# Kernel optimization log

Hardware: AMD Instinct MI355X
Metric: run time of the kernel (lower is better)

Reference implementation:

```python
import jax, jax.numpy as jnp
import numpy as np

N_NODES = 100000
N_EDGES = 3_200_000
F_IN, HID, N_CLS = 512, 16, 16


def setup_inputs() -> dict:
    key = jax.random.key(0)
    k1, k2, k3, k4 = jax.random.split(key, 4)
    x = jax.random.normal(k1, (N_NODES, F_IN), dtype=jnp.float32)
    edge_index = jax.random.randint(k2, (2, N_EDGES), 0, N_NODES, dtype=jnp.int64)
    W1 = jax.random.normal(k3, (F_IN, HID), dtype=jnp.float32) * 0.05
    b1 = jnp.zeros((HID,), dtype=jnp.float32)
    W2 = jax.random.normal(k4, (HID, N_CLS), dtype=jnp.float32) * 0.05
    b2 = jnp.zeros((N_CLS,), dtype=jnp.float32)
    return {"x": x, "edge_index": edge_index, "W1": W1, "b1": b1, "W2": W2, "b2": b2}


def _gcn_conv(x, W, b, row, col, norm, n_nodes):
    # GCNConv: linear first, then symmetric-normalized scatter-add aggregation
    h = x @ W                              # [N, out]
    msg = h[row] * norm[:, None]           # gather + scale, [E+N, out]
    out = jax.ops.segment_sum(msg, col, num_segments=n_nodes)
    return out + b


def reference(x, edge_index, W1, b1, W2, b2):
    n = x.shape[0]
    # add self-loops (GCNConv default)
    loop = jnp.arange(n, dtype=edge_index.dtype)
    row = jnp.concatenate([edge_index[0], loop])
    col = jnp.concatenate([edge_index[1], loop])
    # symmetric normalization D^-1/2 A D^-1/2 with edge_weight = 1
    deg = jax.ops.segment_sum(jnp.ones_like(col, dtype=x.dtype), col, num_segments=n)
    dinv = jnp.where(deg > 0, deg ** -0.5, 0.0)
    norm = dinv[row] * dinv[col]

    h = jax.nn.relu(_gcn_conv(x, W1, b1, row, col, norm, n))
    # dropout is identity in eval mode
    out = _gcn_conv(h, W2, b2, row, col, norm, n)
    return jax.nn.log_softmax(out, axis=-1)
```

## Files before the change

kernel.cpp:

```cpp
#include <hip/hip_runtime.h>
#include <hip/hip_fp16.h>

#define F_IN 512
#define BKT_BITS 7
#define NPB (1 << BKT_BITS)
#define NBMAX 1024
#define BWIN 5120
#define EPT 16
#define EPW (256 * EPT)

__global__ void k_init(int* __restrict__ cursor, int nb) {
    int i = blockIdx.x * blockDim.x + threadIdx.x;
    if (i < nb) cursor[i] = i * BWIN;
}

__global__ __launch_bounds__(256) void k_part(
    const int* __restrict__ row, const int* __restrict__ col,
    int* __restrict__ cursor, unsigned int* __restrict__ pairs, int E, int nb)
{
    __shared__ int hist[NBMAX];
    __shared__ int base[NBMAX];
    int tid = threadIdx.x;
    int e0 = blockIdx.x * EPW;
    for (int i = tid; i < nb; i += 256) hist[i] = 0;
    __syncthreads();
    int4 c4[EPT / 4];
    int rank[EPT];
    #pragma unroll
    for (int k = 0; k < EPT / 4; ++k) {
        int e = e0 + (tid + k * 256) * 4;
        if (e + 3 < E) {
            c4[k] = ((const int4*)col)[e >> 2];
        } else {
            c4[k].x = (e     < E) ? col[e]     : -1;
            c4[k].y = (e + 1 < E) ? col[e + 1] : -1;
            c4[k].z = (e + 2 < E) ? col[e + 2] : -1;
            c4[k].w = (e + 3 < E) ? col[e + 3] : -1;
        }
        const int* cc = (const int*)&c4[k];
        #pragma unroll
        for (int i = 0; i < 4; ++i)
            rank[4 * k + i] = (cc[i] >= 0) ? atomicAdd(&hist[cc[i] >> BKT_BITS], 1) : 0;
    }
    __syncthreads();
    for (int i = tid; i < nb; i += 256)
        base[i] = hist[i] ? atomicAdd(&cursor[i], hist[i]) : 0;
    __syncthreads();
    #pragma unroll
    for (int k = 0; k < EPT / 4; ++k) {
        int e = e0 + (tid + k * 256) * 4;
        int4 r4;
        if (e + 3 < E) {
            r4 = ((const int4*)row)[e >> 2];
        } else {
            r4.x = (e     < E) ? row[e]     : 0;
            r4.y = (e + 1 < E) ? row[e + 1] : 0;
            r4.z = (e + 2 < E) ? row[e + 2] : 0;
            r4.w = (e + 3 < E) ? row[e + 3] : 0;
        }
        const int* cc = (const int*)&c4[k];
        const int* rr = (const int*)&r4;
        #pragma unroll
        for (int i = 0; i < 4; ++i) {
            if (e + i >= E || cc[i] < 0) continue;
            int b = cc[i] >> BKT_BITS;
            int slot = b * BWIN + min(rank[4 * k + i] +
                       (int)0, BWIN - 1);
            slot = b * BWIN;
            int s2 = slot + (base[b] - slot) + rank[4 * k + i];
            if (s2 < (b + 1) * BWIN)
                pairs[s2] = ((unsigned int)rr[i] << BKT_BITS)
                          | (unsigned int)(cc[i] & (NPB - 1));
        }
    }
}

__global__ __launch_bounds__(256) void k_csr(
    unsigned int* __restrict__ pairs, const int* __restrict__ cursor,
    int2* __restrict__ pd, float* __restrict__ dinv, int n, int nb)
{
    __shared__ int hist[NPB];
    __shared__ int sc[NPB];
    __shared__ int curs[NPB];
    int b = blockIdx.x, tid = threadIdx.x;
    int n0 = b << BKT_BITS;
    int w0 = b * BWIN;
    int ec = min(cursor[b] - w0, BWIN);
    if (tid < NPB) hist[tid] = 0;
    __syncthreads();
    uint4 pv4[BWIN / 1024];
    #pragma unroll
    for (int k = 0; k < BWIN / 1024; ++k) {
        pv4[k] = ((const uint4*)(pairs + w0))[tid + k * 256];
        int e = (tid + k * 256) * 4;
        const unsigned int* pp = (const unsigned int*)&pv4[k];
        #pragma unroll
        for (int i = 0; i < 4; ++i)
            if (e + i < ec) atomicAdd(&hist[pp[i] & (NPB - 1)], 1);
    }
    __syncthreads();
    if (tid < NPB) sc[tid] = hist[tid];
    __syncthreads();
    for (int off = 1; off < NPB; off <<= 1) {
        int t = (tid < NPB && tid >= off) ? sc[tid - off] : 0;
        __syncthreads();
        if (tid < NPB) sc[tid] += t;
        __syncthreads();
    }
    if (tid < NPB) {
        int st = sc[tid] - hist[tid];
        curs[tid] = st;
        int node = n0 + tid;
        if (node < n) {
            pd[node] = make_int2(w0 + st, hist[tid]);
            dinv[node] = rsqrtf((float)(hist[tid] + 1));
        }
    }
    __syncthreads();
    #pragma unroll
    for (int k = 0; k < BWIN / 1024; ++k) {
        int e = (tid + k * 256) * 4;
        const unsigned int* pp = (const unsigned int*)&pv4[k];
        #pragma unroll
        for (int i = 0; i < 4; ++i) {
            if (e + i < ec) {
                unsigned int p = pp[i];
                int pos = atomicAdd(&curs[p & (NPB - 1)], 1);
                ((int*)pairs)[w0 + pos] = (int)(p >> BKT_BITS);
            }
        }
    }
}

__global__ __launch_bounds__(256) void k_gemm1(
    const float* __restrict__ x, const float* __restrict__ W1,
    const float* __restrict__ dinv, __half2* __restrict__ hs, int n)
{
    __shared__ float red[4][64 * 17];
    const int lane = threadIdx.x & 63;
    const int wib  = threadIdx.x >> 6;
    const int wave = blockIdx.x * 4 + wib;
    const int nw   = gridDim.x * 4;
    float* rb = red[wib];

    float w[128];
    #pragma unroll
    for (int i = 0; i < 32; ++i) {
        float4 t = ((const float4*)W1)[lane * 32 + i];
        w[4*i+0] = t.x; w[4*i+1] = t.y; w[4*i+2] = t.z; w[4*i+3] = t.w;
    }
    const int q  = lane >> 4;
    const int jj = lane & 15;

    int node = wave;
    float4 a = {}, b = {};
    float di = 0.f;
    if (node < n) {
        const float4* xr = (const float4*)(x + (size_t)node * F_IN);
        a = xr[lane * 2];
        b = xr[lane * 2 + 1];
        di = dinv[node];
    }
    while (node < n) {
        int nxt = node + nw;
        float4 an = {}, bn = {};
        float dn = 0.f;
        if (nxt < n) {
            const float4* xr = (const float4*)(x + (size_t)nxt * F_IN);
            an = xr[lane * 2];
            bn = xr[lane * 2 + 1];
            dn = dinv[nxt];
        }
        float xs[8] = {a.x, a.y, a.z, a.w, b.x, b.y, b.z, b.w};
        float p[16];
        #pragma unroll
        for (int j = 0; j < 16; ++j) p[j] = 0.f;
        #pragma unroll
        for (int i = 0; i < 8; ++i)
            #pragma unroll
            for (int j = 0; j < 16; ++j)
                p[j] = fmaf(xs[i], w[i * 16 + j], p[j]);

        #pragma unroll
        for (int j = 0; j < 16; ++j) rb[lane * 17 + j] = p[j];
        __asm__ volatile("s_waitcnt lgkmcnt(0)" ::: "memory");
        float s = 0.f;
        #pragma unroll
        for (int i = 0; i < 16; ++i) s += rb[(q * 16 + i) * 17 + jj];
        s += __shfl_down(s, 32);
        s += __shfl_down(s, 16);

        float sv = s * di;
        float sn = __shfl_down(sv, 1);
        if (lane < 16 && (lane & 1) == 0) {
            __half2 hv = __halves2half2(__float2half(sv), __float2half(sn));
            hs[node * 8 + (lane >> 1)] = hv;
        }
        node = nxt; a = an; b = bn; di = dn;
    }
}

__global__ __launch_bounds__(256) void k_agg1(
    const __half2* __restrict__ hs, const int2* __restrict__ pd,
    const int* __restrict__ csr, const float* __restrict__ dinv,
    const float* __restrict__ b1, const float* __restrict__ W2,
    __half2* __restrict__ hs2, int n)
{
    int t = blockIdx.x * blockDim.x + threadIdx.x;
    int node = t >> 3, j2 = t & 7;
    if (node >= n) return;
    int2 p = pd[node];
    int e = p.x, s1 = p.x + p.y;
    float2 sum = __half22float2(hs[node * 8 + j2]);
    for (; e + 8 <= s1; e += 8) {
        int a0 = csr[e],   a1 = csr[e+1], a2 = csr[e+2], a3 = csr[e+3];
        int a4 = csr[e+4], a5 = csr[e+5], a6 = csr[e+6], a7 = csr[e+7];
        float2 v0 = __half22float2(hs[a0 * 8 + j2]);
        float2 v1 = __half22float2(hs[a1 * 8 + j2]);
        float2 v2 = __half22float2(hs[a2 * 8 + j2]);
        float2 v3 = __half22float2(hs[a3 * 8 + j2]);
        float2 v4 = __half22float2(hs[a4 * 8 + j2]);
        float2 v5 = __half22float2(hs[a5 * 8 + j2]);
        float2 v6 = __half22float2(hs[a6 * 8 + j2]);
        float2 v7 = __half22float2(hs[a7 * 8 + j2]);
        sum.x += ((v0.x+v1.x)+(v2.x+v3.x)) + ((v4.x+v5.x)+(v6.x+v7.x));
        sum.y += ((v0.y+v1.y)+(v2.y+v3.y)) + ((v4.y+v5.y)+(v6.y+v7.y));
    }
    for (; e < s1; ++e) {
        float2 v = __half22float2(hs[csr[e] * 8 + j2]);
        sum.x += v.x; sum.y += v.y;
    }
    float di = dinv[node];
    float2 b1v = ((const float2*)b1)[j2];
    float va = fmaxf(fmaf(sum.x, di, b1v.x), 0.f);
    float vb = fmaxf(fmaf(sum.y, di, b1v.y), 0.f);
    float ha = 0.f, hb = 0.f;
    #pragma unroll
    for (int k2 = 0; k2 < 8; ++k2) {
        float oa = __shfl(va, k2, 8);
        float ob = __shfl(vb, k2, 8);
        ha = fmaf(oa, W2[(2*k2)   * 16 + 2*j2],     ha);
        hb = fmaf(oa, W2[(2*k2)   * 16 + 2*j2 + 1], hb);
        ha = fmaf(ob, W2[(2*k2+1) * 16 + 2*j2],     ha);
        hb = fmaf(ob, W2[(2*k2+1) * 16 + 2*j2 + 1], hb);
    }
    hs2[node * 8 + j2] = __halves2half2(__float2half(ha * di), __float2half(hb * di));
}

__global__ __launch_bounds__(256) void k_agg2(
    const __half2* __restrict__ hs2, const int2* __restrict__ pd,
    const int* __restrict__ csr, const float* __restrict__ dinv,
    const float* __restrict__ b2, float2* __restrict__ out, int n)
{
    int t = blockIdx.x * blockDim.x + threadIdx.x;
    int node = t >> 3, j2 = t & 7;
    if (node >= n) return;
    int2 p = pd[node];
    int e = p.x, s1 = p.x + p.y;
    float2 sum = __half22float2(hs2[node * 8 + j2]);
    for (; e + 8 <= s1; e += 8) {
        int a0 = csr[e],   a1 = csr[e+1], a2 = csr[e+2], a3 = csr[e+3];
        int a4 = csr[e+4], a5 = csr[e+5], a6 = csr[e+6], a7 = csr[e+7];
        float2 v0 = __half22float2(hs2[a0 * 8 + j2]);
        float2 v1 = __half22float2(hs2[a1 * 8 + j2]);
        float2 v2 = __half22float2(hs2[a2 * 8 + j2]);
        float2 v3 = __half22float2(hs2[a3 * 8 + j2]);
        float2 v4 = __half22float2(hs2[a4 * 8 + j2]);
        float2 v5 = __half22float2(hs2[a5 * 8 + j2]);
        float2 v6 = __half22float2(hs2[a6 * 8 + j2]);
        float2 v7 = __half22float2(hs2[a7 * 8 + j2]);
        sum.x += ((v0.x+v1.x)+(v2.x+v3.x)) + ((v4.x+v5.x)+(v6.x+v7.x));
        sum.y += ((v0.y+v1.y)+(v2.y+v3.y)) + ((v4.y+v5.y)+(v6.y+v7.y));
    }
    for (; e < s1; ++e) {
        float2 v = __half22float2(hs2[csr[e] * 8 + j2]);
        sum.x += v.x; sum.y += v.y;
    }
    float di = dinv[node];
    float2 b2v = ((const float2*)b2)[j2];
    float vx = fmaf(sum.x, di, b2v.x);
    float vy = fmaf(sum.y, di, b2v.y);
    float m = fmaxf(vx, vy);
    #pragma unroll
    for (int off = 4; off >= 1; off >>= 1) m = fmaxf(m, __shfl_xor(m, off));
    float s = expf(vx - m) + expf(vy - m);
    #pragma unroll
    for (int off = 4; off >= 1; off >>= 1) s += __shfl_xor(s, off);
    float ls = logf(s);
    out[node * 8 + j2] = make_float2(vx - m - ls, vy - m - ls);
}

extern "C" void kernel_launch(void* const* d_in, const int* in_sizes, int n_in,
                              void* d_out, int out_size, void* d_ws, size_t ws_size,
                              hipStream_t stream)
{
    const float* x  = (const float*)d_in[0];
    const int*   ei = (const int*)d_in[1];
    const float* W1 = (const float*)d_in[2];
    const float* b1 = (const float*)d_in[3];
    const float* W2 = (const float*)d_in[4];
    const float* b2 = (const float*)d_in[5];
    float* out = (float*)d_out;

    const int n = in_sizes[0] / F_IN;
    const int E = in_sizes[1] / 2;
    const int nb = (n + NPB - 1) >> BKT_BITS;

    char* ws = (char*)d_ws;
    size_t o = 0;
    #define ALIGN512(s) (((s) + 511) & ~(size_t)511)
    float* dinv = (float*)(ws + o);           o += ALIGN512((size_t)n * 4);
    int2*  pd   = (int2*)(ws + o);            o += ALIGN512((size_t)n * 8);
    int*   curs = (int*)(ws + o);             o += ALIGN512((size_t)NBMAX * 4);
    unsigned int* pairs = (unsigned int*)(ws + o);
    o += ALIGN512((size_t)nb * BWIN * 4);
    __half2* hs  = (__half2*)(ws + o);        o += ALIGN512((size_t)n * 16 * 2);
    __half2* hs2 = (__half2*)(ws + o);        o += ALIGN512((size_t)n * 16 * 2);
    #undef ALIGN512

    k_init<<<(nb + 255) / 256, 256, 0, stream>>>(curs, nb);
    k_part<<<(E + EPW - 1) / EPW, 256, 0, stream>>>(ei, ei + E, curs, pairs, E, nb);
    k_csr <<<nb, 256, 0, stream>>>(pairs, curs, pd, dinv, n, nb);

    k_gemm1<<<2048, 256, 0, stream>>>(x, W1, dinv, hs, n);
    k_agg1 <<<(n * 8 + 255) / 256, 256, 0, stream>>>(hs, pd, (const int*)pairs,
                                                     dinv, b1, W2, hs2, n);
    k_agg2 <<<(n * 8 + 255) / 256, 256, 0, stream>>>(hs2, pd, (const int*)pairs,
                                                     dinv, b2, (float2*)out, n);
}
```

Before: 465.5 us.

## Stage partition scatter in LDS and assign a wave per node in aggregation

The partition kernel now processes twice as many edges per block. Each block first sorts its edges by bucket in shared memory using a 1024-entry prefix scan, then writes each bucket's run to global memory as a contiguous span instead of scattering individual words. The CSR kernel builds its sorted window in LDS and writes it back linearly rather than scattering into global memory. Both aggregation kernels now use 64 threads per node, splitting edges across 8 slots and reducing with shuffles. This raises parallelism for the gathers but idles most lanes on low-degree nodes and adds LDS and shuffle overhead.

```diff
diff --git a/kernel.cpp b/kernel.cpp
--- a/kernel.cpp
+++ b/kernel.cpp
@@ -6,7 +6,7 @@
 #define NPB (1 << BKT_BITS)
 #define NBMAX 1024
 #define BWIN 5120
-#define EPT 16
+#define EPT 32
 #define EPW (256 * EPT)
 
 __global__ void k_init(int* __restrict__ cursor, int nb) {
@@ -18,12 +18,16 @@
     const int* __restrict__ row, const int* __restrict__ col,
     int* __restrict__ cursor, unsigned int* __restrict__ pairs, int E, int nb)
 {
+    __shared__ unsigned int staged[EPW];
+    __shared__ unsigned short bkt[EPW];
     __shared__ int hist[NBMAX];
+    __shared__ int sc[NBMAX];
     __shared__ int base[NBMAX];
     int tid = threadIdx.x;
     int e0 = blockIdx.x * EPW;
     for (int i = tid; i < nb; i += 256) hist[i] = 0;
     __syncthreads();
+
     int4 c4[EPT / 4];
     int rank[EPT];
     #pragma unroll
@@ -43,9 +47,23 @@
             rank[4 * k + i] = (cc[i] >= 0) ? atomicAdd(&hist[cc[i] >> BKT_BITS], 1) : 0;
     }
     __syncthreads();
-    for (int i = tid; i < nb; i += 256)
-        base[i] = hist[i] ? atomicAdd(&cursor[i], hist[i]) : 0;
-    __syncthreads();
+
+    for (int i = tid; i < NBMAX; i += 256) {
+        int h = (i < nb) ? hist[i] : 0;
+        base[i] = h ? atomicAdd(&cursor[i], h) : 0;
+        sc[i] = h;
+    }
+    __syncthreads();
+    for (int off = 1; off < NBMAX; off <<= 1) {
+        int t0 = (tid       >= off) ? sc[tid       - off] : 0;
+        int t1 = (tid + 256 >= off) ? sc[tid + 256 - off] : 0;
+        int t2 = (tid + 512 >= off) ? sc[tid + 512 - off] : 0;
+        int t3 = (tid + 768 >= off) ? sc[tid + 768 - off] : 0;
+        __syncthreads();
+        sc[tid] += t0; sc[tid + 256] += t1; sc[tid + 512] += t2; sc[tid + 768] += t3;
+        __syncthreads();
+    }
+
     #pragma unroll
     for (int k = 0; k < EPT / 4; ++k) {
         int e = e0 + (tid + k * 256) * 4;
@@ -64,14 +82,20 @@
         for (int i = 0; i < 4; ++i) {
             if (e + i >= E || cc[i] < 0) continue;
             int b = cc[i] >> BKT_BITS;
-            int slot = b * BWIN + min(rank[4 * k + i] +
-                       (int)0, BWIN - 1);
-            slot = b * BWIN;
-            int s2 = slot + (base[b] - slot) + rank[4 * k + i];
-            if (s2 < (b + 1) * BWIN)
-                pairs[s2] = ((unsigned int)rr[i] << BKT_BITS)
-                          | (unsigned int)(cc[i] & (NPB - 1));
-        }
+            int pos = (sc[b] - hist[b]) + rank[4 * k + i];
+            staged[pos] = ((unsigned int)rr[i] << BKT_BITS)
+                        | (unsigned int)(cc[i] & (NPB - 1));
+            bkt[pos] = (unsigned short)b;
+        }
+    }
+    __syncthreads();
+
+    int vcnt = sc[nb - 1];
+    for (int i = tid; i < vcnt; i += 256) {
+        int b = bkt[i];
+        int gpos = base[b] + (i - (sc[b] - hist[b]));
+        if (gpos < (b + 1) * BWIN)
+            pairs[gpos] = staged[i];
     }
 }
 
@@ -79,6 +103,7 @@
     unsigned int* __restrict__ pairs, const int* __restrict__ cursor,
     int2* __restrict__ pd, float* __restrict__ dinv, int n, int nb)
 {
+    __shared__ int sorted[BWIN];
     __shared__ int hist[NPB];
     __shared__ int sc[NPB];
     __shared__ int curs[NPB];
@@ -88,12 +113,10 @@
     int ec = min(cursor[b] - w0, BWIN);
     if (tid < NPB) hist[tid] = 0;
     __syncthreads();
-    uint4 pv4[BWIN / 1024];
-    #pragma unroll
-    for (int k = 0; k < BWIN / 1024; ++k) {
-        pv4[k] = ((const uint4*)(pairs + w0))[tid + k * 256];
-        int e = (tid + k * 256) * 4;
-        const unsigned int* pp = (const unsigned int*)&pv4[k];
+    for (int e4 = tid; e4 < BWIN / 4; e4 += 256) {
+        uint4 p4 = ((const uint4*)(pairs + w0))[e4];
+        int e = e4 * 4;
+        const unsigned int* pp = (const unsigned int*)&p4;
         #pragma unroll
         for (int i = 0; i < 4; ++i)
             if (e + i < ec) atomicAdd(&hist[pp[i] & (NPB - 1)], 1);
@@ -117,19 +140,22 @@
         }
     }
     __syncthreads();
-    #pragma unroll
-    for (int k = 0; k < BWIN / 1024; ++k) {
-        int e = (tid + k * 256) * 4;
-        const unsigned int* pp = (const unsigned int*)&pv4[k];
+    for (int e4 = tid; e4 < BWIN / 4; e4 += 256) {
+        uint4 p4 = ((const uint4*)(pairs + w0))[e4];
+        int e = e4 * 4;
+        const unsigned int* pp = (const unsigned int*)&p4;
         #pragma unroll
         for (int i = 0; i < 4; ++i) {
             if (e + i < ec) {
                 unsigned int p = pp[i];
                 int pos = atomicAdd(&curs[p & (NPB - 1)], 1);
-                ((int*)pairs)[w0 + pos] = (int)(p >> BKT_BITS);
+                sorted[pos] = (int)(p >> BKT_BITS);
             }
         }
     }
+    __syncthreads();
+    for (int i = tid; i < ec; i += 256)
+        ((int*)pairs)[w0 + i] = sorted[i];
 }
 
 __global__ __launch_bounds__(256) void k_gemm1(
@@ -207,31 +233,26 @@
     __half2* __restrict__ hs2, int n)
 {
     int t = blockIdx.x * blockDim.x + threadIdx.x;
-    int node = t >> 3, j2 = t & 7;
+    int node = t >> 6;
     if (node >= n) return;
+    int l = t & 63, d = l & 7, slot = l >> 3;
     int2 p = pd[node];
-    int e = p.x, s1 = p.x + p.y;
-    float2 sum = __half22float2(hs[node * 8 + j2]);
-    for (; e + 8 <= s1; e += 8) {
-        int a0 = csr[e],   a1 = csr[e+1], a2 = csr[e+2], a3 = csr[e+3];
-        int a4 = csr[e+4], a5 = csr[e+5], a6 = csr[e+6], a7 = csr[e+7];
-        float2 v0 = __half22float2(hs[a0 * 8 + j2]);
-        float2 v1 = __half22float2(hs[a1 * 8 + j2]);
-        float2 v2 = __half22float2(hs[a2 * 8 + j2]);
-        float2 v3 = __half22float2(hs[a3 * 8 + j2]);
-        float2 v4 = __half22float2(hs[a4 * 8 + j2]);
-        float2 v5 = __half22float2(hs[a5 * 8 + j2]);
-        float2 v6 = __half22float2(hs[a6 * 8 + j2]);
-        float2 v7 = __half22float2(hs[a7 * 8 + j2]);
-        sum.x += ((v0.x+v1.x)+(v2.x+v3.x)) + ((v4.x+v5.x)+(v6.x+v7.x));
-        sum.y += ((v0.y+v1.y)+(v2.y+v3.y)) + ((v4.y+v5.y)+(v6.y+v7.y));
-    }
-    for (; e < s1; ++e) {
-        float2 v = __half22float2(hs[csr[e] * 8 + j2]);
-        sum.x += v.x; sum.y += v.y;
-    }
+    float2 sum = make_float2(0.f, 0.f);
+    for (int e = 0; e < p.y; e += 8) {
+        int s = e + slot;
+        bool v = s < p.y;
+        int a = v ? csr[p.x + s] : 0;
+        float2 h = v ? __half22float2(hs[a * 8 + d]) : make_float2(0.f, 0.f);
+        sum.x += h.x; sum.y += h.y;
+    }
+    sum.x += __shfl_xor(sum.x, 8);  sum.y += __shfl_xor(sum.y, 8);
+    sum.x += __shfl_xor(sum.x, 16); sum.y += __shfl_xor(sum.y, 16);
+    sum.x += __shfl_xor(sum.x, 32); sum.y += __shfl_xor(sum.y, 32);
+    float2 self = __half22float2(hs[node * 8 + d]);
+    sum.x += self.x; sum.y += self.y;
+
     float di = dinv[node];
-    float2 b1v = ((const float2*)b1)[j2];
+    float2 b1v = ((const float2*)b1)[d];
     float va = fmaxf(fmaf(sum.x, di, b1v.x), 0.f);
     float vb = fmaxf(fmaf(sum.y, di, b1v.y), 0.f);
     float ha = 0.f, hb = 0.f;
@@ -239,12 +260,13 @@
     for (int k2 = 0; k2 < 8; ++k2) {
         float oa = __shfl(va, k2, 8);
         float ob = __shfl(vb, k2, 8);
-        ha = fmaf(oa, W2[(2*k2)   * 16 + 2*j2],     ha);
-        hb = fmaf(oa, W2[(2*k2)   * 16 + 2*j2 + 1], hb);
-        ha = fmaf(ob, W2[(2*k2+1) * 16 + 2*j2],     ha);
-        hb = fmaf(ob, W2[(2*k2+1) * 16 + 2*j2 + 1], hb);
-    }
-    hs2[node * 8 + j2] = __halves2half2(__float2half(ha * di), __float2half(hb * di));
+        ha = fmaf(oa, W2[(2*k2)   * 16 + 2*d],     ha);
+        hb = fmaf(oa, W2[(2*k2)   * 16 + 2*d + 1], hb);
+        ha = fmaf(ob, W2[(2*k2+1) * 16 + 2*d],     ha);
+        hb = fmaf(ob, W2[(2*k2+1) * 16 + 2*d + 1], hb);
+    }
+    if (l < 8)
+        hs2[node * 8 + d] = __halves2half2(__float2half(ha * di), __float2half(hb * di));
 }
 
 __global__ __launch_bounds__(256) void k_agg2(
@@ -253,41 +275,38 @@
     const float* __restrict__ b2, float2* __restrict__ out, int n)
 {
     int t = blockIdx.x * blockDim.x + threadIdx.x;
-    int node = t >> 3, j2 = t & 7;
+    int node = t >> 6;
     if (node >= n) return;
+    int l = t & 63, d = l & 7, slot = l >> 3;
     int2 p = pd[node];
-    int e = p.x, s1 = p.x + p.y;
-    float2 sum = __half22float2(hs2[node * 8 + j2]);
-    for (; e + 8 <= s1; e += 8) {
-        int a0 = csr[e],   a1 = csr[e+1], a2 = csr[e+2], a3 = csr[e+3];
-        int a4 = csr[e+4], a5 = csr[e+5], a6 = csr[e+6], a7 = csr[e+7];
-        float2 v0 = __half22float2(hs2[a0 * 8 + j2]);
-        float2 v1 = __half22float2(hs2[a1 * 8 + j2]);
-        float2 v2 = __half22float2(hs2[a2 * 8 + j2]);
-        float2 v3 = __half22float2(hs2[a3 * 8 + j2]);
-        float2 v4 = __half22float2(hs2[a4 * 8 + j2]);
-        float2 v5 = __half22float2(hs2[a5 * 8 + j2]);
-        float2 v6 = __half22float2(hs2[a6 * 8 + j2]);
-        float2 v7 = __half22float2(hs2[a7 * 8 + j2]);
-        sum.x += ((v0.x+v1.x)+(v2.x+v3.x)) + ((v4.x+v5.x)+(v6.x+v7.x));
-        sum.y += ((v0.y+v1.y)+(v2.y+v3.y)) + ((v4.y+v5.y)+(v6.y+v7.y));
-    }
-    for (; e < s1; ++e) {
-        float2 v = __half22float2(hs2[csr[e] * 8 + j2]);
-        sum.x += v.x; sum.y += v.y;
-    }
+    float2 sum = make_float2(0.f, 0.f);
+    for (int e = 0; e < p.y; e += 8) {
+        int s = e + slot;
+        bool v = s < p.y;
+        int a = v ? csr[p.x + s] : 0;
+        float2 h = v ? __half22float2(hs2[a * 8 + d]) : make_float2(0.f, 0.f);
+        sum.x += h.x; sum.y += h.y;
+    }
+    sum.x += __shfl_xor(sum.x, 8);  sum.y += __shfl_xor(sum.y, 8);
+    sum.x += __shfl_xor(sum.x, 16); sum.y += __shfl_xor(sum.y, 16);
+    sum.x += __shfl_xor(sum.x, 32); sum.y += __shfl_xor(sum.y, 32);
+    float2 self = __half22float2(hs2[node * 8 + d]);
+    sum.x += self.x; sum.y += self.y;
+
     float di = dinv[node];
-    float2 b2v = ((const float2*)b2)[j2];
+    float2 b2v = ((const float2*)b2)[d];
     float vx = fmaf(sum.x, di, b2v.x);
     float vy = fmaf(sum.y, di, b2v.y);
     float m = fmaxf(vx, vy);
-    #pragma unroll
-    for (int off = 4; off >= 1; off >>= 1) m = fmaxf(m, __shfl_xor(m, off));
+    m = fmaxf(m, __shfl_xor(m, 4));
+    m = fmaxf(m, __shfl_xor(m, 2));
+    m = fmaxf(m, __shfl_xor(m, 1));
     float s = expf(vx - m) + expf(vy - m);
-    #pragma unroll
-    for (int off = 4; off >= 1; off >>= 1) s += __shfl_xor(s, off);
+    s += __shfl_xor(s, 4);
+    s += __shfl_xor(s, 2);
+    s += __shfl_xor(s, 1);
     float ls = logf(s);
-    out[node * 8 + j2] = make_float2(vx - m - ls, vy - m - ls);
+    if (l < 8) out[node * 8 + d] = make_float2(vx - m - ls, vy - m - ls);
 }
 
 extern "C" void kernel_launch(void* const* d_in, const int* in_sizes, int n_in,
@@ -323,8 +342,8 @@
     k_csr <<<nb, 256, 0, stream>>>(pairs, curs, pd, dinv, n, nb);
 
     k_gemm1<<<2048, 256, 0, stream>>>(x, W1, dinv, hs, n);
-    k_agg1 <<<(n * 8 + 255) / 256, 256, 0, stream>>>(hs, pd, (const int*)pairs,
-                                                     dinv, b1, W2, hs2, n);
-    k_agg2 <<<(n * 8 + 255) / 256, 256, 0, stream>>>(hs2, pd, (const int*)pairs,
-                                                     dinv, b2, (float2*)out, n);
-}
+    k_agg1 <<<(n * 64 + 255) / 256, 256, 0, stream>>>(hs, pd, (const int*)pairs,
+                                                      dinv, b1, W2, hs2, n);
+    k_agg2 <<<(n * 64 + 255) / 256, 256, 0, stream>>>(hs2, pd, (const int*)pairs,
+                                                      dinv, b2, (float2*)out, n);
+}
```

Measured after the change: 489.0 us. 5.1% more time.
